# Kernel optimization log

Measured on AMD Instinct MI355X. Metric: run time of the kernel, lower is better.

Reference implementation:

```python
import jax, jax.numpy as jnp
import numpy as np

N_NODES = 50000
N_EDGES = 800000
D_IN = 128
D_OUT = 128


def _gcn_conv(x, W, b, src, dst, num_nodes):
    """PyG GCNConv: h = x @ W^T; symmetric-normalized mean over neighbors
    (with self-loops); out = aggregate + bias.
    src/dst already include self-loops."""
    h = x @ W.T  # [N, C_out]
    ones = jnp.ones(dst.shape[0], dtype=x.dtype)
    deg = jax.ops.segment_sum(ones, dst, num_segments=num_nodes)  # in-degree incl self-loop
    deg_inv_sqrt = jnp.where(deg > 0, jax.lax.rsqrt(deg), 0.0)
    norm = deg_inv_sqrt[src] * deg_inv_sqrt[dst]  # [E+N]
    msgs = h[src] * norm[:, None]  # gather + scale
    out = jax.ops.segment_sum(msgs, dst, num_segments=num_nodes)  # scatter-add
    return out + b


def setup_inputs() -> dict:
    key = jax.random.key(0)
    ks = jax.random.split(key, 9)
    x_r1 = jax.random.normal(ks[0], (N_NODES, D_IN), dtype=jnp.float32)
    x_r2 = jax.random.normal(ks[1], (N_NODES, D_IN), dtype=jnp.float32)
    x_i1 = jax.random.normal(ks[2], (N_NODES, D_IN), dtype=jnp.float32)
    x_i2 = jax.random.normal(ks[3], (N_NODES, D_IN), dtype=jnp.float32)
    edge_index = jax.random.randint(ks[4], (2, N_EDGES), 0, N_NODES, dtype=jnp.int64)
    s = 1.0 / np.sqrt(D_IN)
    W1 = jax.random.uniform(ks[5], (D_OUT, D_IN), minval=-s, maxval=s, dtype=jnp.float32)
    W2 = jax.random.uniform(ks[6], (D_OUT, D_IN), minval=-s, maxval=s, dtype=jnp.float32)
    b1 = jax.random.uniform(ks[7], (D_OUT,), minval=-s, maxval=s, dtype=jnp.float32)
    b2 = jax.random.uniform(ks[8], (D_OUT,), minval=-s, maxval=s, dtype=jnp.float32)
    return {"x_r1": x_r1, "x_r2": x_r2, "x_i1": x_i1, "x_i2": x_i2,
            "edge_index": edge_index, "W1": W1, "b1": b1, "W2": W2, "b2": b2}


def reference(x_r1, x_r2, x_i1, x_i2, edge_index, W1, b1, W2, b2):
    num_nodes = x_r1.shape[0]
    loops = jnp.arange(num_nodes, dtype=edge_index.dtype)
    src = jnp.concatenate([edge_index[0], loops])  # add self-loops
    dst = jnp.concatenate([edge_index[1], loops])
    # real1/imag1 share (W1, b1); real2/imag2 share (W2, b2)
    h_r1 = _gcn_conv(x_r1, W1, b1, src, dst, num_nodes)
    h_r2 = _gcn_conv(x_r2, W2, b2, src, dst, num_nodes)
    h_i1 = _gcn_conv(x_i1, W1, b1, src, dst, num_nodes)
    h_i2 = _gcn_conv(x_i2, W2, b2, src, dst, num_nodes)
    return (h_r1, h_r2, h_i1, h_i2)
```

## Files before the change

kernel.cpp:

```cpp
#include <hip/hip_runtime.h>

#define DD 128

typedef __bf16 bf16x8 __attribute__((ext_vector_type(8)));
typedef float f32x4 __attribute__((ext_vector_type(4)));

static __device__ __forceinline__ unsigned short f2bf(float f) {
    unsigned int u = __float_as_uint(f);
    u += 0x7FFF + ((u >> 16) & 1);
    return (unsigned short)(u >> 16);
}
static __device__ __forceinline__ float bf2f(unsigned short v) {
    return __uint_as_float(((unsigned)v) << 16);
}


__global__ void k_zero(int* __restrict__ p, int n) {
    int i = blockIdx.x * 256 + threadIdx.x;
    if (i < n) p[i] = 0;
}

__global__ void k_count(const int* __restrict__ dst, int* __restrict__ cnt, int E) {
    int e = blockIdx.x * 256 + threadIdx.x;
    if (e < E) atomicAdd(&cnt[dst[e]], 1);
}

__global__ __launch_bounds__(1024) void k_scan1(const int* __restrict__ cnt,
                                                int* __restrict__ rp,
                                                float* __restrict__ dinv,
                                                int* __restrict__ bsum, int N) {
    __shared__ int wsum[16];
    const int tid = threadIdx.x, lane = tid & 63, wid = tid >> 6;
    const int i = blockIdx.x * 1024 + tid;
    int v = (i < N) ? cnt[i] : 0;
    int s = v;
    for (int off = 1; off < 64; off <<= 1) {
        int t = __shfl_up(s, off, 64);
        if (lane >= off) s += t;
    }
    if (lane == 63) wsum[wid] = s;
    __syncthreads();
    int woff = 0, total = 0;
#pragma unroll
    for (int w2 = 0; w2 < 16; ++w2) {
        int t = wsum[w2];
        if (w2 < wid) woff += t;
        total += t;
    }
    if (i < N) {
        rp[i + 1] = woff + s;
        dinv[i] = rsqrtf((float)(v + 1));
    }
    if (tid == 0) bsum[blockIdx.x] = total;
}

__global__ __launch_bounds__(1024) void k_scan2(const int* __restrict__ bsum,
                                                int* __restrict__ rp, int N) {
    __shared__ int boff_s;
    const int tid = threadIdx.x;
    if (tid < 64) {
        int v = (tid < (int)blockIdx.x) ? bsum[tid] : 0;
        for (int off = 32; off > 0; off >>= 1) v += __shfl_down(v, off, 64);
        if (tid == 0) boff_s = v;
    }
    __syncthreads();
    const int i = blockIdx.x * 1024 + tid;
    if (i < N) rp[i + 1] += boff_s;
    if (i == 0) rp[0] = 0;
}

__global__ void k_fill(const int* __restrict__ ei, const int* __restrict__ rp,
                       int* __restrict__ cnt, int* __restrict__ csr, int E) {
    int e = blockIdx.x * 256 + threadIdx.x;
    if (e >= E) return;
    int s = ei[e], d = ei[E + e];
    int old = atomicSub(&cnt[d], 1);
    csr[rp[d] + old - 1] = s;
}


__global__ __launch_bounds__(256) void k_gemm(
    const float* __restrict__ x0, const float* __restrict__ x1,
    const float* __restrict__ x2, const float* __restrict__ x3,
    const float* __restrict__ W1, const float* __restrict__ W2,
    unsigned short* __restrict__ h, int N)
{
    const int m = blockIdx.y;
    const float* x = (m == 0) ? x0 : (m == 1) ? x1 : (m == 2) ? x2 : x3;
    const float* W = (m & 1) ? W2 : W1;

    __shared__ unsigned short Ws[128 * 128];
    __shared__ unsigned short ts[64 * 136];

    const int tid = threadIdx.x;
    const int n0 = blockIdx.x * 64;

    for (int t = tid; t < 128 * 128 / 4; t += 256) {
        float4 v = ((const float4*)W)[t];
        ushort4 b;
        b.x = f2bf(v.x); b.y = f2bf(v.y); b.z = f2bf(v.z); b.w = f2bf(v.w);
        *(ushort4*)&Ws[t * 4] = b;
    }
    for (int t = tid; t < 64 * 32; t += 256) {
        int r = t >> 5;
        int n = n0 + r;
        float4 v = make_float4(0.f, 0.f, 0.f, 0.f);
        if (n < N) v = ((const float4*)(x + (size_t)n * DD))[t & 31];
        ushort4 b;
        b.x = f2bf(v.x); b.y = f2bf(v.y); b.z = f2bf(v.z); b.w = f2bf(v.w);
        *(ushort4*)&ts[r * 128 + (t & 31) * 4] = b;
    }
    __syncthreads();

    const int w    = tid >> 6;
    const int lane = tid & 63;
    const int am   = lane & 15;
    const int aq   = lane >> 4;
    const int r0   = w * 16;

    f32x4 acc[8] = {};
#pragma unroll
    for (int kk = 0; kk < 128; kk += 32) {
        bf16x8 af = *(const bf16x8*)&ts[(r0 + am) * 128 + kk + aq * 8];
#pragma unroll
        for (int ct = 0; ct < 8; ++ct) {
            bf16x8 bf = *(const bf16x8*)&Ws[(ct * 16 + am) * 128 + kk + aq * 8];
            acc[ct] = __builtin_amdgcn_mfma_f32_16x16x32_bf16(af, bf, acc[ct], 0, 0, 0);
        }
    }
    __syncthreads();

    const int cc = lane & 15;
    const int rr = (lane >> 4) * 4;
#pragma unroll
    for (int ct = 0; ct < 8; ++ct)
#pragma unroll
        for (int i = 0; i < 4; ++i)
            ts[(r0 + rr + i) * 136 + ct * 16 + cc] = f2bf(acc[ct][i]);
    __syncthreads();

#pragma unroll
    for (int k = 0; k < 4; ++k) {
        int f = k * 256 + tid;
        int row = f >> 4, ch = f & 15;
        int n = n0 + row;
        if (n < N) {
            uint4 v = *(const uint4*)&ts[row * 136 + ch * 8];
            *(uint4*)(h + ((size_t)n * 4 + m) * DD + ch * 8) = v;
        }
    }
}


__global__ __launch_bounds__(256) void k_gather(
    const int* __restrict__ rp, const int* __restrict__ csr,
    const float* __restrict__ dinv, const unsigned short* __restrict__ h,
    const float* __restrict__ b1, const float* __restrict__ b2,
    float* __restrict__ out, int N)
{
    const int n   = blockIdx.x;
    const int tid = threadIdx.x;
    const int p   = tid >> 7;
    const int idx = tid & 127;
    const int m   = idx >> 5;
    const int c   = (idx & 31) * 4;
    const size_t off = (size_t)idx * 4;

    const float dn = dinv[n];
    float ax = 0.f, ay = 0.f, az = 0.f, aw = 0.f;

    if (p == 0) {
        const float sn = dn * dn;
        const float* bb = (m & 1) ? b2 : b1;
        ushort4 hv = *(const ushort4*)(h + (size_t)n * 512 + off);
        float4 bv = *(const float4*)(bb + c);
        ax = bf2f(hv.x) * sn + bv.x; ay = bf2f(hv.y) * sn + bv.y;
        az = bf2f(hv.z) * sn + bv.z; aw = bf2f(hv.w) * sn + bv.w;
    }

    const int j0 = rp[n], j1 = rp[n + 1];
    const int half = (j1 - j0 + 1) >> 1;
    int jb = j0 + p * half;
    const int je = p ? j1 : (j0 + half);

    for (; jb + 3 < je; jb += 4) {
        int s0 = csr[jb], s1 = csr[jb + 1], s2 = csr[jb + 2], s3 = csr[jb + 3];
        float w0 = dinv[s0] * dn, w1 = dinv[s1] * dn,
              w2 = dinv[s2] * dn, w3 = dinv[s3] * dn;
        ushort4 v0 = *(const ushort4*)(h + (size_t)s0 * 512 + off);
        ushort4 v1 = *(const ushort4*)(h + (size_t)s1 * 512 + off);
        ushort4 v2 = *(const ushort4*)(h + (size_t)s2 * 512 + off);
        ushort4 v3 = *(const ushort4*)(h + (size_t)s3 * 512 + off);
        ax += bf2f(v0.x) * w0 + bf2f(v1.x) * w1 + bf2f(v2.x) * w2 + bf2f(v3.x) * w3;
        ay += bf2f(v0.y) * w0 + bf2f(v1.y) * w1 + bf2f(v2.y) * w2 + bf2f(v3.y) * w3;
        az += bf2f(v0.z) * w0 + bf2f(v1.z) * w1 + bf2f(v2.z) * w2 + bf2f(v3.z) * w3;
        aw += bf2f(v0.w) * w0 + bf2f(v1.w) * w1 + bf2f(v2.w) * w2 + bf2f(v3.w) * w3;
    }
    for (; jb < je; ++jb) {
        int s0 = csr[jb];
        float wgt = dinv[s0] * dn;
        ushort4 v = *(const ushort4*)(h + (size_t)s0 * 512 + off);
        ax += bf2f(v.x) * wgt; ay += bf2f(v.y) * wgt;
        az += bf2f(v.z) * wgt; aw += bf2f(v.w) * wgt;
    }

    __shared__ float part[512];
    if (p == 1) *(float4*)&part[idx * 4] = make_float4(ax, ay, az, aw);
    __syncthreads();
    if (p == 0) {
        float4 t = *(const float4*)&part[idx * 4];
        f32x4 r;
        r.x = ax + t.x; r.y = ay + t.y; r.z = az + t.z; r.w = aw + t.w;
        __builtin_nontemporal_store(r, (f32x4*)(out + ((size_t)m * N + n) * DD + c));
    }
}


extern "C" void kernel_launch(void* const* d_in, const int* in_sizes, int n_in,
                              void* d_out, int out_size, void* d_ws, size_t ws_size,
                              hipStream_t stream) {
    const float* x0 = (const float*)d_in[0];
    const float* x1 = (const float*)d_in[1];
    const float* x2 = (const float*)d_in[2];
    const float* x3 = (const float*)d_in[3];
    const int*   ei = (const int*)d_in[4];
    const float* W1 = (const float*)d_in[5];
    const float* b1 = (const float*)d_in[6];
    const float* W2 = (const float*)d_in[7];
    const float* b2 = (const float*)d_in[8];
    float* out = (float*)d_out;

    const int N = in_sizes[0] / DD;
    const int E = in_sizes[4] / 2;

    int*   cnt  = (int*)d_ws;
    int*   rp   = cnt + 65536;
    float* dinv = (float*)(rp + 65536);
    int*   bsum = (int*)(dinv + 65536);
    int*   csr  = bsum + 256;
    unsigned short* h = (unsigned short*)(csr + E);

    const int nb = (N + 1023) / 1024;

    k_zero <<<(N + 255) / 256, 256, 0, stream>>>(cnt, N);
    k_count<<<(E + 255) / 256, 256, 0, stream>>>(ei + E, cnt, E);
    k_scan1<<<nb, 1024, 0, stream>>>(cnt, rp, dinv, bsum, N);
    k_scan2<<<nb, 1024, 0, stream>>>(bsum, rp, N);
    k_fill <<<(E + 255) / 256, 256, 0, stream>>>(ei, rp, cnt, csr, E);

    dim3 g((N + 63) / 64, 4);
    k_gemm<<<g, 256, 0, stream>>>(x0, x1, x2, x3, W1, W2, h, N);

    k_gather<<<N, 256, 0, stream>>>(rp, csr, dinv, h, b1, b2, out, N);
}
```

Before: 439.6 us.

## Fuse CSR build into one persistent kernel and widen gather to four waves

```diff
diff --git a/kernel.cpp b/kernel.cpp
--- a/kernel.cpp
+++ b/kernel.cpp
@@ -15,67 +15,79 @@
 }
 
 
-__global__ void k_zero(int* __restrict__ p, int n) {
-    int i = blockIdx.x * 256 + threadIdx.x;
-    if (i < n) p[i] = 0;
-}
-
-__global__ void k_count(const int* __restrict__ dst, int* __restrict__ cnt, int E) {
-    int e = blockIdx.x * 256 + threadIdx.x;
-    if (e < E) atomicAdd(&cnt[dst[e]], 1);
-}
-
-__global__ __launch_bounds__(1024) void k_scan1(const int* __restrict__ cnt,
-                                                int* __restrict__ rp,
-                                                float* __restrict__ dinv,
-                                                int* __restrict__ bsum, int N) {
-    __shared__ int wsum[16];
-    const int tid = threadIdx.x, lane = tid & 63, wid = tid >> 6;
-    const int i = blockIdx.x * 1024 + tid;
-    int v = (i < N) ? cnt[i] : 0;
-    int s = v;
-    for (int off = 1; off < 64; off <<= 1) {
-        int t = __shfl_up(s, off, 64);
-        if (lane >= off) s += t;
-    }
-    if (lane == 63) wsum[wid] = s;
-    __syncthreads();
-    int woff = 0, total = 0;
-#pragma unroll
-    for (int w2 = 0; w2 < 16; ++w2) {
-        int t = wsum[w2];
-        if (w2 < wid) woff += t;
-        total += t;
-    }
-    if (i < N) {
-        rp[i + 1] = woff + s;
-        dinv[i] = rsqrtf((float)(v + 1));
-    }
-    if (tid == 0) bsum[blockIdx.x] = total;
-}
-
-__global__ __launch_bounds__(1024) void k_scan2(const int* __restrict__ bsum,
-                                                int* __restrict__ rp, int N) {
-    __shared__ int boff_s;
-    const int tid = threadIdx.x;
-    if (tid < 64) {
-        int v = (tid < (int)blockIdx.x) ? bsum[tid] : 0;
-        for (int off = 32; off > 0; off >>= 1) v += __shfl_down(v, off, 64);
-        if (tid == 0) boff_s = v;
-    }
-    __syncthreads();
-    const int i = blockIdx.x * 1024 + tid;
-    if (i < N) rp[i + 1] += boff_s;
-    if (i == 0) rp[0] = 0;
-}
-
-__global__ void k_fill(const int* __restrict__ ei, const int* __restrict__ rp,
-                       int* __restrict__ cnt, int* __restrict__ csr, int E) {
-    int e = blockIdx.x * 256 + threadIdx.x;
-    if (e >= E) return;
-    int s = ei[e], d = ei[E + e];
-    int old = atomicSub(&cnt[d], 1);
-    csr[rp[d] + old - 1] = s;
+static __device__ __forceinline__ void gbar(int* ctr, int target) {
+    __syncthreads();
+    if (threadIdx.x == 0) {
+        __hip_atomic_fetch_add(ctr, 1, __ATOMIC_ACQ_REL, __HIP_MEMORY_SCOPE_AGENT);
+        while (__hip_atomic_load(ctr, __ATOMIC_ACQUIRE, __HIP_MEMORY_SCOPE_AGENT) < target)
+            __builtin_amdgcn_s_sleep(2);
+    }
+    __syncthreads();
+}
+
+__global__ __launch_bounds__(1024) void k_build(
+    const int* __restrict__ ei, int* __restrict__ cnt, int* __restrict__ rp,
+    float* __restrict__ dinv, int* __restrict__ bsum, int2* __restrict__ csr,
+    int* __restrict__ bar, int N, int E, int nscan)
+{
+    const int tid  = threadIdx.x;
+    const int bid  = blockIdx.x;
+    const int nblk = gridDim.x;
+    const int gsz  = nblk * 1024;
+
+    for (int e = bid * 1024 + tid; e < E; e += gsz)
+        atomicAdd(&cnt[ei[E + e]], 1);
+
+    gbar(&bar[0], nblk);
+
+    if (bid < nscan) {
+        __shared__ int wsum[16];
+        const int lane = tid & 63, wid = tid >> 6;
+        const int i = bid * 1024 + tid;
+        int v = (i < N) ? cnt[i] : 0;
+        int s = v;
+        for (int off = 1; off < 64; off <<= 1) {
+            int t = __shfl_up(s, off, 64);
+            if (lane >= off) s += t;
+        }
+        if (lane == 63) wsum[wid] = s;
+        __syncthreads();
+        int woff = 0, total = 0;
+#pragma unroll
+        for (int w2 = 0; w2 < 16; ++w2) {
+            int t = wsum[w2];
+            if (w2 < wid) woff += t;
+            total += t;
+        }
+        if (i < N) {
+            rp[i + 1] = woff + s;
+            dinv[i] = rsqrtf((float)(v + 1));
+        }
+        if (tid == 0) bsum[bid] = total;
+    }
+
+    gbar(&bar[1], nblk);
+
+    if (bid < nscan) {
+        __shared__ int boff_s;
+        if (tid < 64) {
+            int v = (tid < bid) ? bsum[tid] : 0;
+            for (int off = 32; off > 0; off >>= 1) v += __shfl_down(v, off, 64);
+            if (tid == 0) boff_s = v;
+        }
+        __syncthreads();
+        const int i = bid * 1024 + tid;
+        if (i < N) rp[i + 1] += boff_s;
+        if (i == 0) rp[0] = 0;
+    }
+
+    gbar(&bar[2], nblk);
+
+    for (int e = bid * 1024 + tid; e < E; e += gsz) {
+        int s = ei[e], d = ei[E + e];
+        int old = atomicSub(&cnt[d], 1);
+        csr[rp[d] + old - 1] = make_int2(s, __float_as_int(dinv[s]));
+    }
 }
 
 
@@ -152,66 +164,84 @@
 }
 
 
+static __device__ __forceinline__ void acc8(float* a, uint4 v, float wt) {
+    a[0] += __uint_as_float(v.x << 16) * wt;
+    a[1] += __uint_as_float(v.x & 0xffff0000u) * wt;
+    a[2] += __uint_as_float(v.y << 16) * wt;
+    a[3] += __uint_as_float(v.y & 0xffff0000u) * wt;
+    a[4] += __uint_as_float(v.z << 16) * wt;
+    a[5] += __uint_as_float(v.z & 0xffff0000u) * wt;
+    a[6] += __uint_as_float(v.w << 16) * wt;
+    a[7] += __uint_as_float(v.w & 0xffff0000u) * wt;
+}
+
 __global__ __launch_bounds__(256) void k_gather(
-    const int* __restrict__ rp, const int* __restrict__ csr,
+    const int* __restrict__ rp, const int2* __restrict__ csr,
     const float* __restrict__ dinv, const unsigned short* __restrict__ h,
     const float* __restrict__ b1, const float* __restrict__ b2,
     float* __restrict__ out, int N)
 {
-    const int n   = blockIdx.x;
-    const int tid = threadIdx.x;
-    const int p   = tid >> 7;
-    const int idx = tid & 127;
-    const int m   = idx >> 5;
-    const int c   = (idx & 31) * 4;
-    const size_t off = (size_t)idx * 4;
+    const int n    = blockIdx.x;
+    const int tid  = threadIdx.x;
+    const int w    = tid >> 6;
+    const int lane = tid & 63;
+    const int m    = lane >> 4;
+    const int c    = (lane & 15) * 8;
+    const size_t off = (size_t)lane * 8;
 
     const float dn = dinv[n];
-    float ax = 0.f, ay = 0.f, az = 0.f, aw = 0.f;
-
-    if (p == 0) {
+    float a[8] = {};
+
+    if (w == 3) {
         const float sn = dn * dn;
         const float* bb = (m & 1) ? b2 : b1;
-        ushort4 hv = *(const ushort4*)(h + (size_t)n * 512 + off);
-        float4 bv = *(const float4*)(bb + c);
-        ax = bf2f(hv.x) * sn + bv.x; ay = bf2f(hv.y) * sn + bv.y;
-        az = bf2f(hv.z) * sn + bv.z; aw = bf2f(hv.w) * sn + bv.w;
+        uint4 hv = *(const uint4*)(h + (size_t)n * 512 + off);
+        acc8(a, hv, sn);
+        float4 bv0 = *(const float4*)(bb + c);
+        float4 bv1 = *(const float4*)(bb + c + 4);
+        a[0] += bv0.x; a[1] += bv0.y; a[2] += bv0.z; a[3] += bv0.w;
+        a[4] += bv1.x; a[5] += bv1.y; a[6] += bv1.z; a[7] += bv1.w;
     }
 
     const int j0 = rp[n], j1 = rp[n + 1];
-    const int half = (j1 - j0 + 1) >> 1;
-    int jb = j0 + p * half;
-    const int je = p ? j1 : (j0 + half);
+    const int q  = (j1 - j0 + 3) >> 2;
+    int jb = j0 + w * q;
+    int je = jb + q; if (je > j1) je = j1;
 
     for (; jb + 3 < je; jb += 4) {
-        int s0 = csr[jb], s1 = csr[jb + 1], s2 = csr[jb + 2], s3 = csr[jb + 3];
-        float w0 = dinv[s0] * dn, w1 = dinv[s1] * dn,
-              w2 = dinv[s2] * dn, w3 = dinv[s3] * dn;
-        ushort4 v0 = *(const ushort4*)(h + (size_t)s0 * 512 + off);
-        ushort4 v1 = *(const ushort4*)(h + (size_t)s1 * 512 + off);
-        ushort4 v2 = *(const ushort4*)(h + (size_t)s2 * 512 + off);
-        ushort4 v3 = *(const ushort4*)(h + (size_t)s3 * 512 + off);
-        ax += bf2f(v0.x) * w0 + bf2f(v1.x) * w1 + bf2f(v2.x) * w2 + bf2f(v3.x) * w3;
-        ay += bf2f(v0.y) * w0 + bf2f(v1.y) * w1 + bf2f(v2.y) * w2 + bf2f(v3.y) * w3;
-        az += bf2f(v0.z) * w0 + bf2f(v1.z) * w1 + bf2f(v2.z) * w2 + bf2f(v3.z) * w3;
-        aw += bf2f(v0.w) * w0 + bf2f(v1.w) * w1 + bf2f(v2.w) * w2 + bf2f(v3.w) * w3;
+        int2 e0 = csr[jb], e1 = csr[jb + 1], e2 = csr[jb + 2], e3 = csr[jb + 3];
+        float w0 = __int_as_float(e0.y) * dn, w1 = __int_as_float(e1.y) * dn,
+              w2 = __int_as_float(e2.y) * dn, w3 = __int_as_float(e3.y) * dn;
+        uint4 v0 = *(const uint4*)(h + (size_t)e0.x * 512 + off);
+        uint4 v1 = *(const uint4*)(h + (size_t)e1.x * 512 + off);
+        uint4 v2 = *(const uint4*)(h + (size_t)e2.x * 512 + off);
+        uint4 v3 = *(const uint4*)(h + (size_t)e3.x * 512 + off);
+        acc8(a, v0, w0); acc8(a, v1, w1); acc8(a, v2, w2); acc8(a, v3, w3);
     }
     for (; jb < je; ++jb) {
-        int s0 = csr[jb];
-        float wgt = dinv[s0] * dn;
-        ushort4 v = *(const ushort4*)(h + (size_t)s0 * 512 + off);
-        ax += bf2f(v.x) * wgt; ay += bf2f(v.y) * wgt;
-        az += bf2f(v.z) * wgt; aw += bf2f(v.w) * wgt;
-    }
-
-    __shared__ float part[512];
-    if (p == 1) *(float4*)&part[idx * 4] = make_float4(ax, ay, az, aw);
-    __syncthreads();
-    if (p == 0) {
-        float4 t = *(const float4*)&part[idx * 4];
-        f32x4 r;
-        r.x = ax + t.x; r.y = ay + t.y; r.z = az + t.z; r.w = aw + t.w;
-        __builtin_nontemporal_store(r, (f32x4*)(out + ((size_t)m * N + n) * DD + c));
+        int2 e = csr[jb];
+        float wt = __int_as_float(e.y) * dn;
+        uint4 v = *(const uint4*)(h + (size_t)e.x * 512 + off);
+        acc8(a, v, wt);
+    }
+
+    __shared__ float part[3][64][8];
+    if (w) {
+        *(f32x4*)&part[w - 1][lane][0] = *(f32x4*)&a[0];
+        *(f32x4*)&part[w - 1][lane][4] = *(f32x4*)&a[4];
+    }
+    __syncthreads();
+    if (w == 0) {
+#pragma unroll
+        for (int k = 0; k < 3; ++k)
+#pragma unroll
+            for (int i = 0; i < 8; ++i) a[i] += part[k][lane][i];
+        float* po = out + ((size_t)m * N + n) * DD + c;
+        f32x4 r0, r1;
+        r0.x = a[0]; r0.y = a[1]; r0.z = a[2]; r0.w = a[3];
+        r1.x = a[4]; r1.y = a[5]; r1.z = a[6]; r1.w = a[7];
+        __builtin_nontemporal_store(r0, (f32x4*)po);
+        __builtin_nontemporal_store(r1, (f32x4*)(po + 4));
     }
 }
 
@@ -234,19 +264,18 @@
     const int E = in_sizes[4] / 2;
 
     int*   cnt  = (int*)d_ws;
-    int*   rp   = cnt + 65536;
+    int*   bar  = cnt + 65536;
+    int*   rp   = bar + 64;
     float* dinv = (float*)(rp + 65536);
     int*   bsum = (int*)(dinv + 65536);
-    int*   csr  = bsum + 256;
+    int2*  csr  = (int2*)(bsum + 256);
     unsigned short* h = (unsigned short*)(csr + E);
 
-    const int nb = (N + 1023) / 1024;
-
-    k_zero <<<(N + 255) / 256, 256, 0, stream>>>(cnt, N);
-    k_count<<<(E + 255) / 256, 256, 0, stream>>>(ei + E, cnt, E);
-    k_scan1<<<nb, 1024, 0, stream>>>(cnt, rp, dinv, bsum, N);
-    k_scan2<<<nb, 1024, 0, stream>>>(bsum, rp, N);
-    k_fill <<<(E + 255) / 256, 256, 0, stream>>>(ei, rp, cnt, csr, E);
+    const int nscan = (N + 1023) / 1024;
+    const int nblk  = 256;
+
+    hipMemsetAsync(cnt, 0, (65536 + 64) * sizeof(int), stream);
+    k_build<<<nblk, 1024, 0, stream>>>(ei, cnt, rp, dinv, bsum, csr, bar, N, E, nscan);
 
     dim3 g((N + 63) / 64, 4);
     k_gemm<<<g, 256, 0, stream>>>(x0, x1, x2, x3, W1, W2, h, N);
```

After: 474.0 us. +7.8%, slower.
